# Kernel tuning notes

Measured on AMD Instinct MI355X. Metric: run time of the kernel, lower is better.

Reference implementation:

```python
import jax, jax.numpy as jnp
import numpy as np

NUM_CLASSES = 1000
CHANNELS = 256
N = 4096
EPS = 1e-8  # torch F.cosine_similarity eps


def setup_inputs() -> dict:
    key = jax.random.key(0)
    k1, k2 = jax.random.split(key)
    x = jax.random.normal(k1, (N, CHANNELS), dtype=jnp.float32)
    class_logits = jax.random.normal(k2, (N, NUM_CLASSES), dtype=jnp.float32)
    return {"x": x, "class_logits": class_logits}


def reference(x, class_logits):
    # class_logits.clone().detach()
    logits = jax.lax.stop_gradient(class_logits)
    pred_normed = jax.nn.softmax(logits, axis=1)
    max_logit = jnp.max(pred_normed, axis=1)          # computed (unused downstream), faithful
    max_cls = jnp.argmax(pred_normed, axis=1)         # [N]

    # graph(): pairwise cosine similarity [N, N] without materializing [N, N, D]
    norms = jnp.linalg.norm(x, axis=1)                # [N]
    dots = x @ x.T                                    # [N, N]
    mat = dots / jnp.maximum(norms[:, None] * norms[None, :], EPS)

    # aggregation
    x_aggregation = mat @ x + x                       # [N, D]
    x_new = jax.lax.stop_gradient(x_aggregation)      # .clone().detach()

    # update_prototype: scatter-add then mean per class (vectorized scatter)
    sums = jax.ops.segment_sum(x_new, max_cls, num_segments=NUM_CLASSES)           # [C, D]
    counts = jax.ops.segment_sum(jnp.ones((x.shape[0],), x.dtype), max_cls,
                                 num_segments=NUM_CLASSES)                          # [C]
    exist = counts[:, None] > 0
    prototypes = jnp.where(exist, sums / jnp.maximum(counts[:, None], 1.0), 0.0)    # [C, D]

    # inter-class difference matrix: p1 - p2 -> inter[i, j] = protos[j] - protos[i]
    inter_class_matrix = prototypes[None, :, :] - prototypes[:, None, :]            # [C, C, D]
    return prototypes, inter_class_matrix
```

## Files before the change

### kernel.cpp

```cpp
#include <hip/hip_runtime.h>
#include <math.h>

#define N 4096
#define C 256
#define NC 1000

typedef float v4f __attribute__((ext_vector_type(4)));

__global__ __launch_bounds__(256) void k_norm(const float* __restrict__ x,
                                              float* __restrict__ inv_n) {
    int w = threadIdx.x >> 6, lane = threadIdx.x & 63;
    int row = blockIdx.x * 4 + w;
    const float4* x4 = (const float4*)(x + row * C);
    float4 v = x4[lane];
    float s = v.x * v.x + v.y * v.y + v.z * v.z + v.w * v.w;
    #pragma unroll
    for (int off = 32; off; off >>= 1) s += __shfl_xor(s, off, 64);
    if (lane == 0) inv_n[row] = (s > 0.f) ? 1.0f / sqrtf(s) : 0.f;
}

__global__ __launch_bounds__(256) void k_argmax(const float* __restrict__ logits,
                                                int* __restrict__ cls) {
    int w = threadIdx.x >> 6, lane = threadIdx.x & 63;
    int row = blockIdx.x * 4 + w;
    const float* L = logits + (long)row * NC;
    float best = -3.402823466e38f;
    int bi = 0;
    #pragma unroll
    for (int k = 0; k < 16; k++) {
        int idx = lane + 64 * k;
        if (idx < NC) {
            float v = L[idx];
            if (v > best) { best = v; bi = idx; }
        }
    }
    #pragma unroll
    for (int off = 32; off; off >>= 1) {
        float ov = __shfl_xor(best, off, 64);
        int   oi = __shfl_xor(bi, off, 64);
        if (ov > best || (ov == best && oi < bi)) { best = ov; bi = oi; }
    }
    if (lane == 0) cls[row] = bi;
}

__global__ __launch_bounds__(256) void k_zpart(const float* __restrict__ x,
                                               const float* __restrict__ inv_n,
                                               float* __restrict__ part) {
    __shared__ float As[32][64];
    __shared__ float Bs[32][64];
    int t = threadIdx.x;
    int tx = t & 15, ty = t >> 4;
    int a0 = blockIdx.x * 64, b0 = blockIdx.y * 64;
    int k0 = blockIdx.z * 256;
    float acc[4][4] = {};
    for (int kk = 0; kk < 256; kk += 32) {
        #pragma unroll
        for (int r = 0; r < 8; r++) {
            int idx = r * 256 + t;
            int il = idx >> 6, col = idx & 63;
            int gi = k0 + kk + il;
            float wv = inv_n[gi];
            As[il][col] = x[gi * C + a0 + col] * wv;
            Bs[il][col] = x[gi * C + b0 + col];
        }
        __syncthreads();
        #pragma unroll 8
        for (int il = 0; il < 32; il++) {
            float4 a4 = *(const float4*)&As[il][4 * ty];
            float4 b4 = *(const float4*)&Bs[il][4 * tx];
            acc[0][0] += a4.x * b4.x; acc[0][1] += a4.x * b4.y; acc[0][2] += a4.x * b4.z; acc[0][3] += a4.x * b4.w;
            acc[1][0] += a4.y * b4.x; acc[1][1] += a4.y * b4.y; acc[1][2] += a4.y * b4.z; acc[1][3] += a4.y * b4.w;
            acc[2][0] += a4.z * b4.x; acc[2][1] += a4.z * b4.y; acc[2][2] += a4.z * b4.z; acc[2][3] += a4.z * b4.w;
            acc[3][0] += a4.w * b4.x; acc[3][1] += a4.w * b4.y; acc[3][2] += a4.w * b4.z; acc[3][3] += a4.w * b4.w;
        }
        __syncthreads();
    }
    float* P = part + (long)blockIdx.z * (C * C);
    #pragma unroll
    for (int p = 0; p < 4; p++)
        #pragma unroll
        for (int q = 0; q < 4; q++)
            P[(a0 + 4 * ty + p) * C + (b0 + 4 * tx + q)] = acc[p][q];
}

__global__ __launch_bounds__(256) void k_zreduce(const float* __restrict__ part,
                                                 float* __restrict__ Z) {
    int i = blockIdx.x * 256 + threadIdx.x;
    float s = 0.f;
    #pragma unroll
    for (int k = 0; k < 16; k++) s += part[k * (C * C) + i];
    Z[i] = s;
}

__global__ __launch_bounds__(256) void k_agg(const float* __restrict__ x,
                                             const float* __restrict__ Z,
                                             const float* __restrict__ inv_n,
                                             float* __restrict__ xn) {
    __shared__ float xs[4][C];
    int w = threadIdx.x >> 6, lane = threadIdx.x & 63;
    int row = blockIdx.x * 4 + w;
    const float4* xr4 = (const float4*)(x + row * C);
    float4 xv = xr4[lane];
    *(float4*)&xs[w][4 * lane] = xv;
    __syncthreads();
    float4 acc = {0.f, 0.f, 0.f, 0.f};
    const float4* Z4 = (const float4*)Z;
    #pragma unroll 8
    for (int a = 0; a < C; a++) {
        float s = xs[w][a];
        float4 z = Z4[a * 64 + lane];
        acc.x += s * z.x; acc.y += s * z.y; acc.z += s * z.z; acc.w += s * z.w;
    }
    float inv = inv_n[row];
    acc.x = acc.x * inv + xv.x;
    acc.y = acc.y * inv + xv.y;
    acc.z = acc.z * inv + xv.z;
    acc.w = acc.w * inv + xv.w;
    ((float4*)(xn + row * C))[lane] = acc;
}

__global__ __launch_bounds__(256) void k_proto(const float* __restrict__ xn,
                                               const int* __restrict__ cls,
                                               float* __restrict__ proto) {
    __shared__ int cl[N];
    int t = threadIdx.x, c = blockIdx.x;
    #pragma unroll
    for (int k = 0; k < N; k += 256) cl[k + t] = cls[k + t];
    __syncthreads();
    float acc = 0.f;
    int cnt = 0;
    for (int i = 0; i < N; i++) {
        if (cl[i] == c) { acc += xn[i * C + t]; cnt++; }
    }
    proto[c * C + t] = cnt ? acc / (float)cnt : 0.f;
}

__global__ __launch_bounds__(256) void k_inter(const float* __restrict__ proto,
                                               float* __restrict__ out) {
    int w = threadIdx.x >> 6, lane = threadIdx.x & 63;
    int ib = blockIdx.x % 250, jc = blockIdx.x / 250;
    int i = ib * 4 + w;
    int j0 = jc * 250;
    const v4f* p4 = (const v4f*)proto;
    v4f pi = p4[i * 64 + lane];
    v4f* o4 = (v4f*)out;
    for (int j = j0; j < j0 + 250; j++) {
        v4f pj = p4[j * 64 + lane];
        v4f d = pj - pi;
        __builtin_nontemporal_store(d, &o4[((long)i * NC + j) * 64 + lane]);
    }
}

extern "C" void kernel_launch(void* const* d_in, const int* in_sizes, int n_in,
                              void* d_out, int out_size, void* d_ws, size_t ws_size,
                              hipStream_t stream) {
    const float* x      = (const float*)d_in[0];
    const float* logits = (const float*)d_in[1];

    float* ws    = (float*)d_ws;
    float* inv_n = ws;
    int*   cls   = (int*)(ws + 4096);
    float* Z     = ws + 8192;
    float* part  = ws + 73728;
    float* xn    = part;

    float* proto = (float*)d_out;
    float* inter = (float*)d_out + NC * C;

    k_norm  <<<1024, 256, 0, stream>>>(x, inv_n);
    k_argmax<<<1024, 256, 0, stream>>>(logits, cls);
    k_zpart <<<dim3(4, 4, 16), 256, 0, stream>>>(x, inv_n, part);
    k_zreduce<<<C * C / 256, 256, 0, stream>>>(part, Z);
    k_agg   <<<1024, 256, 0, stream>>>(x, Z, inv_n, xn);
    k_proto <<<NC, 256, 0, stream>>>(xn, cls, proto);
    k_inter <<<1000, 256, 0, stream>>>(proto, inter);
}
```

Measured before the change: 1.303 ms.

## Use ballot bitmasks in prototype kernel, 2-row aggregation, finer inter-class grid

The prototype kernel no longer scans all 4096 class labels serially per block. It builds a 64-word ballot bitmask of the rows matching its class and visits only the set bits, which removes the long serial loop over labels. The aggregation kernel now handles 8 rows per block (2 per wavefront), so each Z load is reused across two rows. The inter-class kernel uses a 2D grid of 250x8 blocks with 125 columns each, which gives more parallelism for the large output write.

```diff
diff --git a/kernel.cpp b/kernel.cpp
--- a/kernel.cpp
+++ b/kernel.cpp
@@ -6,6 +6,10 @@
 #define NC 1000
 
 typedef float v4f __attribute__((ext_vector_type(4)));
+
+static __device__ __forceinline__ v4f splat4(float s) {
+    v4f r; r.x = s; r.y = s; r.z = s; r.w = s; return r;
+}
 
 __global__ __launch_bounds__(256) void k_norm(const float* __restrict__ x,
                                               float* __restrict__ inv_n) {
@@ -96,41 +100,60 @@
                                              const float* __restrict__ Z,
                                              const float* __restrict__ inv_n,
                                              float* __restrict__ xn) {
-    __shared__ float xs[4][C];
-    int w = threadIdx.x >> 6, lane = threadIdx.x & 63;
-    int row = blockIdx.x * 4 + w;
-    const float4* xr4 = (const float4*)(x + row * C);
-    float4 xv = xr4[lane];
-    *(float4*)&xs[w][4 * lane] = xv;
+    __shared__ float xs[8][C];
+    int t = threadIdx.x;
+    int w = t >> 6, lane = t & 63;
+    int r0 = blockIdx.x * 8;
+    #pragma unroll
+    for (int q = 0; q < 2; q++) {
+        int idx = q * 256 + t;
+        int row = idx >> 6, col4 = idx & 63;
+        *(float4*)&xs[row][col4 * 4] = ((const float4*)(x + (long)(r0 + row) * C))[col4];
+    }
     __syncthreads();
-    float4 acc = {0.f, 0.f, 0.f, 0.f};
-    const float4* Z4 = (const float4*)Z;
+    int wr = w * 2;
+    v4f acc[2] = {};
+    const v4f* Z4 = (const v4f*)Z;
     #pragma unroll 8
     for (int a = 0; a < C; a++) {
-        float s = xs[w][a];
-        float4 z = Z4[a * 64 + lane];
-        acc.x += s * z.x; acc.y += s * z.y; acc.z += s * z.z; acc.w += s * z.w;
+        v4f z = Z4[a * 64 + lane];
+        #pragma unroll
+        for (int r = 0; r < 2; r++)
+            acc[r] += splat4(xs[wr + r][a]) * z;
     }
-    float inv = inv_n[row];
-    acc.x = acc.x * inv + xv.x;
-    acc.y = acc.y * inv + xv.y;
-    acc.z = acc.z * inv + xv.z;
-    acc.w = acc.w * inv + xv.w;
-    ((float4*)(xn + row * C))[lane] = acc;
+    #pragma unroll
+    for (int r = 0; r < 2; r++) {
+        int row = r0 + wr + r;
+        float inv = inv_n[row];
+        v4f xv = *(const v4f*)&xs[wr + r][lane * 4];
+        v4f res = acc[r] * splat4(inv) + xv;
+        *(v4f*)(xn + (long)row * C + lane * 4) = res;
+    }
 }
 
 __global__ __launch_bounds__(256) void k_proto(const float* __restrict__ xn,
                                                const int* __restrict__ cls,
                                                float* __restrict__ proto) {
-    __shared__ int cl[N];
+    __shared__ unsigned long long bits[64];
     int t = threadIdx.x, c = blockIdx.x;
+    int w = t >> 6, lane = t & 63;
     #pragma unroll
-    for (int k = 0; k < N; k += 256) cl[k + t] = cls[k + t];
+    for (int k = 0; k < 16; k++) {
+        int wd = w * 16 + k;
+        unsigned long long m = __ballot(cls[wd * 64 + lane] == c);
+        if (lane == 0) bits[wd] = m;
+    }
     __syncthreads();
     float acc = 0.f;
     int cnt = 0;
-    for (int i = 0; i < N; i++) {
-        if (cl[i] == c) { acc += xn[i * C + t]; cnt++; }
+    for (int wd = 0; wd < 64; wd++) {
+        unsigned long long m = bits[wd];
+        cnt += __popcll(m);
+        while (m) {
+            int b = __ffsll((long long)m) - 1;
+            m &= m - 1;
+            acc += xn[(long)(wd * 64 + b) * C + t];
+        }
     }
     proto[c * C + t] = cnt ? acc / (float)cnt : 0.f;
 }
@@ -138,16 +161,15 @@
 __global__ __launch_bounds__(256) void k_inter(const float* __restrict__ proto,
                                                float* __restrict__ out) {
     int w = threadIdx.x >> 6, lane = threadIdx.x & 63;
-    int ib = blockIdx.x % 250, jc = blockIdx.x / 250;
-    int i = ib * 4 + w;
-    int j0 = jc * 250;
+    int i = blockIdx.x * 4 + w;
+    int j0 = blockIdx.y * 125;
     const v4f* p4 = (const v4f*)proto;
     v4f pi = p4[i * 64 + lane];
-    v4f* o4 = (v4f*)out;
-    for (int j = j0; j < j0 + 250; j++) {
+    v4f* o4 = (v4f*)out + (long)i * NC * 64 + lane;
+    #pragma unroll 5
+    for (int j = j0; j < j0 + 125; j++) {
         v4f pj = p4[j * 64 + lane];
-        v4f d = pj - pi;
-        __builtin_nontemporal_store(d, &o4[((long)i * NC + j) * 64 + lane]);
+        __builtin_nontemporal_store(pj - pi, &o4[(long)j * 64]);
     }
 }
 
@@ -167,11 +189,11 @@
     float* proto = (float*)d_out;
     float* inter = (float*)d_out + NC * C;
 
-    k_norm  <<<1024, 256, 0, stream>>>(x, inv_n);
-    k_argmax<<<1024, 256, 0, stream>>>(logits, cls);
-    k_zpart <<<dim3(4, 4, 16), 256, 0, stream>>>(x, inv_n, part);
+    k_norm   <<<1024, 256, 0, stream>>>(x, inv_n);
+    k_argmax <<<1024, 256, 0, stream>>>(logits, cls);
+    k_zpart  <<<dim3(4, 4, 16), 256, 0, stream>>>(x, inv_n, part);
     k_zreduce<<<C * C / 256, 256, 0, stream>>>(part, Z);
-    k_agg   <<<1024, 256, 0, stream>>>(x, Z, inv_n, xn);
-    k_proto <<<NC, 256, 0, stream>>>(xn, cls, proto);
-    k_inter <<<1000, 256, 0, stream>>>(proto, inter);
+    k_agg    <<<512, 256, 0, stream>>>(x, Z, inv_n, xn);
+    k_proto  <<<NC, 256, 0, stream>>>(xn, cls, proto);
+    k_inter  <<<dim3(250, 8), 256, 0, stream>>>(proto, inter);
 }
```

New measurement: 1.098 ms. -15.8%, faster.
